# Optimization experiments

Hardware: AMD Instinct MI355X
Metric: run time of the kernel (lower is better)

## Reference

```python
import jax, jax.numpy as jnp
import numpy as np

# Planck radiance in wavenumber form: B(nu, T) = c1*nu^3 / (exp(c2*nu/T) - 1)
# nu in cm^-1, T in Kelvin, B in W / (m^2 sr cm^-1)
C1 = 1.191042e-8
C2 = 1.4387752
N_TEMPS = 20


def planck_radiance(nu, T):
    return C1 * nu ** 3 / jnp.expm1(C2 * nu / T)


def setup_inputs() -> dict:
    key = jax.random.key(0)
    k1, k2, k3 = jax.random.split(key, 3)
    N, C = 1048576, 54  # 1024x1024 pixels, 54 spectral channels
    wg = jnp.linspace(720.0, 1250.0, C, dtype=jnp.float32)
    v = (wg - wg.min()) / (wg.max() - wg.min())
    pi = 3.14159
    library = jnp.stack([
        jnp.full((C,), 0.98),                      # skin
        0.9 + 0.05 * jnp.sin(2 * pi * v),          # fabric_cotton
        0.15 + 0.1 * v,                            # metal_aluminum
        0.95 - 0.03 * v,                           # vegetation
        0.92 + 0.02 * jnp.sin(4 * pi * v),         # concrete
        0.85 + 0.1 * v,                            # glass
    ]).astype(jnp.float32)
    # realistic LWIR radiance magnitudes (~0.02-0.12 W/m^2/sr/cm^-1)
    s_sky = 0.05 * jax.random.uniform(k1, (C,), dtype=jnp.float32)
    s_ground = 0.08 + 0.02 * jax.random.uniform(k2, (C,), dtype=jnp.float32)
    s_obs = 0.02 + 0.1 * jax.random.uniform(k3, (N, C), dtype=jnp.float32)
    return {"s_obs": s_obs, "s_sky": s_sky, "s_ground": s_ground,
            "library": library, "wavenumber_grid": wg}


def reference(s_obs, s_sky, s_ground, library, wavenumber_grid):
    N, C = s_obs.shape
    M = library.shape[0]
    t_cand = jnp.linspace(250.0, 350.0, N_TEMPS, dtype=s_obs.dtype)
    # All candidate model spectra are pixel-independent (V fixed at 0.5):
    x_amb = 0.5 * s_sky + 0.5 * s_ground                           # [C]
    B = planck_radiance(wavenumber_grid[None, :], t_cand[:, None])  # [T, C]
    s_model = library[:, None, :] * B[None, :, :] \
        + (1.0 - library[:, None, :]) * x_amb                       # [M, T, C]
    cand = s_model.reshape(M * N_TEMPS, C)  # row-major: idx = m*T + t, matches loop order
    # ||s_obs - cand||^2 expanded: memory-bound [N, M*T] loss matrix
    losses = (jnp.sum(s_obs ** 2, axis=-1, keepdims=True)
              - 2.0 * s_obs @ cand.T
              + jnp.sum(cand ** 2, axis=-1))                        # [N, M*T]
    best = jnp.argmin(losses, axis=-1)                              # first-min, matches strict '<'
    best_loss = jnp.take_along_axis(losses, best[:, None], axis=1)[:, 0]
    m_idx = best // N_TEMPS
    t_idx = best % N_TEMPS
    best_t = t_cand[t_idx]                                          # [N]
    best_e = library[m_idx]                                         # [N, C]
    best_v = jnp.full((N,), 0.5, dtype=s_obs.dtype)
    s_recon = best_e * planck_radiance(wavenumber_grid[None, :], best_t[:, None]) \
        + (1.0 - best_e) * x_amb                                    # [N, C]
    texture = best_e.mean(axis=-1)
    beta = jnp.zeros((N, 1), dtype=s_obs.dtype)
    objective = best_loss.mean()
    return (best_t, best_e, best_v, beta, texture, s_recon, objective)
```

## Files before the change

### kernel.cpp

```cpp
#include <hip/hip_runtime.h>
#include <math.h>

#define C_CH 54
#define CP   64
#define NT   20
#define NM   6
#define NK   120
#define BLK  256

typedef float sf16 __attribute__((ext_vector_type(16)));
typedef float sf8  __attribute__((ext_vector_type(8)));

__global__ __launch_bounds__(256) void hadar_prep(
    const float* __restrict__ s_sky, const float* __restrict__ s_ground,
    const float* __restrict__ library, const float* __restrict__ wg,
    float* __restrict__ cand)
{
    __shared__ float xamb[C_CH];
    __shared__ float tc[NT];
    __shared__ float lm[NM];
    const int tid = threadIdx.x;
    if (tid < NT) tc[tid] = 250.0f + (float)tid * (100.0f / 19.0f);
    if (tid < C_CH) xamb[tid] = 0.5f * s_sky[tid] + 0.5f * s_ground[tid];
    if (tid < NM) {
        float s = 0.0f;
        for (int c = 0; c < C_CH; ++c) s += library[tid * C_CH + c];
        lm[tid] = s / (float)C_CH;
    }
    __syncthreads();

    const float c1 = 1.191042e-8f, c2 = 1.4387752f;
    for (int idx = tid; idx < NK * CP; idx += 256) {
        const int k = idx >> 6, c = idx & 63;
        float v = 0.0f;
        if (c < C_CH) {
            const int m = k / NT, t = k - m * NT;
            const float nu = wg[c];
            const float B = c1 * nu * nu * nu / expm1f(c2 * nu / tc[t]);
            const float e = library[m * C_CH + c];
            v = e * B + (1.0f - e) * xamb[c];
        }
        cand[idx] = v;
    }
    __syncthreads();

    if (tid < NK) {
        float s = 0.0f;
        for (int c = 0; c < C_CH; ++c) { float v = cand[tid * CP + c]; s += v * v; }
        const int m = tid / NT, t = tid - m * NT;
        cand[tid * CP + 54] = s;
        cand[tid * CP + 55] = tc[t];
        cand[tid * CP + 56] = lm[m];
    }
}

#define CE(c) ((c) < 16 ? q0[(c)] : (c) < 32 ? q1[(c)-16] : (c) < 48 ? q2[(c)-32] : q3[(c)-48])

__global__ __launch_bounds__(BLK) void hadar_main(
    const float* __restrict__ s_obs,
    const float* __restrict__ library,
    const float* __restrict__ cand,
    float* __restrict__ out, float* __restrict__ partials, int N)
{
    const int tid = threadIdx.x;
    const long long n0 = (long long)blockIdx.x * BLK + tid;
    const bool v0 = (n0 < N);

    float row0[C_CH];
    if (v0) {
        const float2* rp = (const float2*)(s_obs + n0 * C_CH);
        #pragma unroll
        for (int i = 0; i < C_CH / 2; ++i) {
            float2 w = rp[i];
            row0[2 * i] = w.x; row0[2 * i + 1] = w.y;
        }
    } else {
        #pragma unroll
        for (int c = 0; c < C_CH; ++c) row0[c] = 0.0f;
    }

    float ssq0 = 0.0f;
    #pragma unroll
    for (int c = 0; c < C_CH; ++c) ssq0 += row0[c] * row0[c];

    float bl0 = 3.4e38f;
    int bk0 = NK;

    const int wid = __builtin_amdgcn_readfirstlane(tid >> 6);
    const int rot = (int)((blockIdx.x * 4u + (unsigned)wid) % 15u) * 8;

    int kk = rot;
    const float* pk = cand + (size_t)rot * CP;
    #pragma unroll 1
    for (int i = 0; i < NK; ++i) {
        sf16 q0, q1, q2;
        sf8  q3;
        asm volatile("s_load_dwordx16 %0, %1, 0x0"  : "=s"(q0) : "s"(pk));
        asm volatile("s_load_dwordx16 %0, %1, 0x40" : "=s"(q1) : "s"(pk));
        asm volatile("s_load_dwordx16 %0, %1, 0x80" : "=s"(q2) : "s"(pk));
        asm volatile("s_load_dwordx8  %0, %1, 0xc0" : "=s"(q3) : "s"(pk));
        asm volatile("s_waitcnt lgkmcnt(0)" : "+s"(q0), "+s"(q1), "+s"(q2), "+s"(q3));

        float a0[4] = {0.f, 0.f, 0.f, 0.f};
        #pragma unroll
        for (int c = 0; c < C_CH; ++c) {
            a0[c & 3] += row0[c] * CE(c);
        }
        const float sq = q3[6];
        const float d0 = (a0[0] + a0[1]) + (a0[2] + a0[3]);
        const float l0 = (ssq0 - 2.0f * d0) + sq;
        if (l0 < bl0 || (l0 == bl0 && kk < bk0)) { bl0 = l0; bk0 = kk; }

        ++kk; pk += CP;
        if (kk == NK) { kk = 0; pk = cand; }
    }

    const size_t NN = (size_t)N;
    const size_t NC = (size_t)C_CH * NN;
    float lsum = 0.0f;

    if (v0) {
        lsum = bl0;
        const int m = bk0 / NT;
        const float* crow = cand + (size_t)bk0 * CP;

        out[n0] = crow[55];
        out[NN + NC + n0] = 0.5f;
        out[2 * NN + NC + n0] = 0.0f;
        out[3 * NN + NC + n0] = crow[56];

        float2* bep = (float2*)(out + NN + (size_t)n0 * C_CH);
        const float2* lp = (const float2*)(library + m * C_CH);
        #pragma unroll
        for (int i = 0; i < C_CH / 2; ++i) bep[i] = lp[i];

        float2* srp = (float2*)(out + 4 * NN + NC + (size_t)n0 * C_CH);
        const float2* cp2 = (const float2*)crow;
        #pragma unroll
        for (int i = 0; i < C_CH / 2; ++i) srp[i] = cp2[i];
    }

    __shared__ float red[BLK];
    red[tid] = lsum;
    __syncthreads();
    #pragma unroll
    for (int s = BLK / 2; s > 0; s >>= 1) {
        if (tid < s) red[tid] += red[tid + s];
        __syncthreads();
    }
    if (tid == 0) partials[blockIdx.x] = red[0];
}

__global__ __launch_bounds__(256) void hadar_reduce(
    const float* __restrict__ partials, int nb, float* __restrict__ obj_out, float invN)
{
    __shared__ float red[256];
    float s = 0.0f;
    for (int i = threadIdx.x; i < nb; i += 256) s += partials[i];
    red[threadIdx.x] = s;
    __syncthreads();
    #pragma unroll
    for (int st = 128; st > 0; st >>= 1) {
        if (threadIdx.x < st) red[threadIdx.x] += red[threadIdx.x + st];
        __syncthreads();
    }
    if (threadIdx.x == 0) *obj_out = red[0] * invN;
}

extern "C" void kernel_launch(void* const* d_in, const int* in_sizes, int n_in,
                              void* d_out, int out_size, void* d_ws, size_t ws_size,
                              hipStream_t stream)
{
    const float* s_obs    = (const float*)d_in[0];
    const float* s_sky    = (const float*)d_in[1];
    const float* s_ground = (const float*)d_in[2];
    const float* library  = (const float*)d_in[3];
    const float* wg       = (const float*)d_in[4];
    float* out = (float*)d_out;

    const int N  = in_sizes[0] / C_CH;
    const int nb = (N + BLK - 1) / BLK;

    float* ws       = (float*)d_ws;
    float* cand     = ws;
    float* partials = ws + 8192;

    hadar_prep<<<1, 256, 0, stream>>>(s_sky, s_ground, library, wg, cand);
    hadar_main<<<nb, BLK, 0, stream>>>(s_obs, library, cand, out, partials, N);

    const size_t NN = (size_t)N;
    float* obj_out = out + 4 * NN + 2 * (size_t)C_CH * NN;
    hadar_reduce<<<1, 256, 0, stream>>>(partials, nb, obj_out, 1.0f / (float)N);
}
```

Measured before the change: 764.9 us.

## Process two pixels per thread and coalesce per-channel output writes via shared indices

Each thread now handles two pixels, so every scalar-loaded candidate row feeds two dot products and the scalar-load and wait cost per loaded row is amortized. The per-pixel emissivity and reconstruction writes are moved from per-thread strided float2 stores to a block-cooperative loop that writes consecutive addresses, using best indices staged in shared memory. This raises register pressure (two 54-float rows) and halves the grid, which may lower occupancy.

```diff
diff --git a/kernel.cpp b/kernel.cpp
--- a/kernel.cpp
+++ b/kernel.cpp
@@ -7,6 +7,8 @@
 #define NM   6
 #define NK   120
 #define BLK  256
+#define PPT  2
+#define PIX_PER_BLK (BLK * PPT)
 
 typedef float sf16 __attribute__((ext_vector_type(16)));
 typedef float sf8  __attribute__((ext_vector_type(8)));
@@ -63,10 +65,13 @@
     float* __restrict__ out, float* __restrict__ partials, int N)
 {
     const int tid = threadIdx.x;
-    const long long n0 = (long long)blockIdx.x * BLK + tid;
+    const long long base = (long long)blockIdx.x * PIX_PER_BLK;
+    const long long n0 = base + tid;
+    const long long n1 = base + BLK + tid;
     const bool v0 = (n0 < N);
-
-    float row0[C_CH];
+    const bool v1 = (n1 < N);
+
+    float row0[C_CH], row1[C_CH];
     if (v0) {
         const float2* rp = (const float2*)(s_obs + n0 * C_CH);
         #pragma unroll
@@ -78,13 +83,26 @@
         #pragma unroll
         for (int c = 0; c < C_CH; ++c) row0[c] = 0.0f;
     }
-
-    float ssq0 = 0.0f;
+    if (v1) {
+        const float2* rp = (const float2*)(s_obs + n1 * C_CH);
+        #pragma unroll
+        for (int i = 0; i < C_CH / 2; ++i) {
+            float2 w = rp[i];
+            row1[2 * i] = w.x; row1[2 * i + 1] = w.y;
+        }
+    } else {
+        #pragma unroll
+        for (int c = 0; c < C_CH; ++c) row1[c] = 0.0f;
+    }
+
+    float ssq0 = 0.0f, ssq1 = 0.0f;
     #pragma unroll
     for (int c = 0; c < C_CH; ++c) ssq0 += row0[c] * row0[c];
-
-    float bl0 = 3.4e38f;
-    int bk0 = NK;
+    #pragma unroll
+    for (int c = 0; c < C_CH; ++c) ssq1 += row1[c] * row1[c];
+
+    float bl0 = 3.4e38f, bl1 = 3.4e38f;
+    int bk0 = NK, bk1 = NK;
 
     const int wid = __builtin_amdgcn_readfirstlane(tid >> 6);
     const int rot = (int)((blockIdx.x * 4u + (unsigned)wid) % 15u) * 8;
@@ -102,42 +120,67 @@
         asm volatile("s_waitcnt lgkmcnt(0)" : "+s"(q0), "+s"(q1), "+s"(q2), "+s"(q3));
 
         float a0[4] = {0.f, 0.f, 0.f, 0.f};
+        float a1[4] = {0.f, 0.f, 0.f, 0.f};
         #pragma unroll
         for (int c = 0; c < C_CH; ++c) {
-            a0[c & 3] += row0[c] * CE(c);
+            const float ce = CE(c);
+            a0[c & 3] += row0[c] * ce;
+            a1[c & 3] += row1[c] * ce;
         }
         const float sq = q3[6];
         const float d0 = (a0[0] + a0[1]) + (a0[2] + a0[3]);
+        const float d1 = (a1[0] + a1[1]) + (a1[2] + a1[3]);
         const float l0 = (ssq0 - 2.0f * d0) + sq;
+        const float l1 = (ssq1 - 2.0f * d1) + sq;
         if (l0 < bl0 || (l0 == bl0 && kk < bk0)) { bl0 = l0; bk0 = kk; }
+        if (l1 < bl1 || (l1 == bl1 && kk < bk1)) { bl1 = l1; bk1 = kk; }
 
         ++kk; pk += CP;
         if (kk == NK) { kk = 0; pk = cand; }
     }
 
+    if (!v0) bk0 = 0;
+    if (!v1) bk1 = 0;
+
     const size_t NN = (size_t)N;
     const size_t NC = (size_t)C_CH * NN;
-    float lsum = 0.0f;
 
     if (v0) {
-        lsum = bl0;
-        const int m = bk0 / NT;
-        const float* crow = cand + (size_t)bk0 * CP;
-
-        out[n0] = crow[55];
+        const float* cr = cand + (size_t)bk0 * CP;
+        out[n0] = cr[55];
         out[NN + NC + n0] = 0.5f;
         out[2 * NN + NC + n0] = 0.0f;
-        out[3 * NN + NC + n0] = crow[56];
-
-        float2* bep = (float2*)(out + NN + (size_t)n0 * C_CH);
-        const float2* lp = (const float2*)(library + m * C_CH);
-        #pragma unroll
-        for (int i = 0; i < C_CH / 2; ++i) bep[i] = lp[i];
-
-        float2* srp = (float2*)(out + 4 * NN + NC + (size_t)n0 * C_CH);
-        const float2* cp2 = (const float2*)crow;
-        #pragma unroll
-        for (int i = 0; i < C_CH / 2; ++i) srp[i] = cp2[i];
+        out[3 * NN + NC + n0] = cr[56];
+    }
+    if (v1) {
+        const float* cr = cand + (size_t)bk1 * CP;
+        out[n1] = cr[55];
+        out[NN + NC + n1] = 0.5f;
+        out[2 * NN + NC + n1] = 0.0f;
+        out[3 * NN + NC + n1] = cr[56];
+    }
+
+    __shared__ int2 bkm[PIX_PER_BLK];
+    bkm[tid]       = make_int2(bk0 * CP, (bk0 / NT) * C_CH);
+    bkm[tid + BLK] = make_int2(bk1 * CP, (bk1 / NT) * C_CH);
+
+    float lsum = (v0 ? bl0 : 0.0f) + (v1 ? bl1 : 0.0f);
+    __syncthreads();
+
+    {
+        float* __restrict__ be = out + NN + (size_t)base * C_CH;
+        float* __restrict__ sr = out + 4 * NN + NC + (size_t)base * C_CH;
+        int p = tid / C_CH;
+        int c = tid - p * C_CH;
+        #pragma unroll 4
+        for (int j = tid; j < PIX_PER_BLK * C_CH; j += BLK) {
+            const int2 o = bkm[p];
+            const float ev = library[o.y + c];
+            const float sv = cand[o.x + c];
+            if (base + p < N) { be[j] = ev; sr[j] = sv; }
+            p += 4; c += 40;
+            if (c >= C_CH) { c -= C_CH; ++p; }
+        }
     }
 
     __shared__ float red[BLK];
@@ -179,7 +222,7 @@
     float* out = (float*)d_out;
 
     const int N  = in_sizes[0] / C_CH;
-    const int nb = (N + BLK - 1) / BLK;
+    const int nb = (N + PIX_PER_BLK - 1) / PIX_PER_BLK;
 
     float* ws       = (float*)d_ws;
     float* cand     = ws;
```

Measured after the change: 777.4 us. No clear change (+1.6%).
